# Optimization experiments

Measured on AMD Instinct MI355X. Metric: run time of the kernel, lower is better.

## Reference

```python
import jax, jax.numpy as jnp
import numpy as np

CUTOFF = 5.0
NLINKED = 1
CELL_LIST = CUTOFF / NLINKED  # linked-cell edge length
_r = np.arange(-NLINKED, NLINKED + 1)
# torch.cartesian_prod(r1,r1,r1) == meshgrid(indexing='ij') stacked & flattened
LINKED = np.stack(np.meshgrid(_r, _r, _r, indexing='ij'), axis=-1).reshape(1, -1, 3).astype(np.float32)  # (1, 27, 3)


def setup_inputs() -> dict:
    N = 2744
    L = 30.0
    key = jax.random.key(0)
    k1, k2 = jax.random.split(key)
    coordinates = jax.random.uniform(k1, (N, 3), dtype=jnp.float32) * L
    cell = jnp.eye(3, dtype=jnp.float32) * L
    mass = jax.random.uniform(k2, (N,), dtype=jnp.float32) * 15.0 + 1.0
    period_table = jnp.ones((3,), dtype=jnp.int32)  # fully periodic
    return {"period_table": period_table, "coordinates": coordinates, "cell": cell, "mass": mass}


def _forward(period_table, coordinates, cell, mass):
    numatom = coordinates.shape[0]
    # wrap coordinates into the cell relative to atom 0 (fractional coords)
    inv_cell = jnp.linalg.inv(cell)
    inv_coor = coordinates @ inv_cell
    inv_coor = inv_coor - jnp.round(inv_coor - inv_coor[0])
    coordinates = inv_coor @ cell
    # remove center of mass
    com = (mass @ coordinates) / jnp.sum(mass)
    coordinates = coordinates - com[None, :]
    # periodic replicas needed to cover the cutoff
    num_repeats = jnp.ceil(jnp.min(CUTOFF / jnp.abs(cell), axis=0)).astype(jnp.int32)
    num_repeats = period_table.astype(jnp.int32) * num_repeats
    up = num_repeats + 1
    down = -num_repeats
    rs = [jnp.arange(int(down[i]), int(up[i])) for i in range(3)]
    g = jnp.meshgrid(*rs, indexing='ij')
    shifts_frac = jnp.stack(g, axis=-1).reshape(-1, 3).astype(coordinates.dtype)  # (S, 3)
    shifts = shifts_frac @ cell  # (S, 3) cartesian shift vectors
    num_shifts = shifts.shape[0]
    # prod = cartesian_prod(all_shifts, all_atoms).T : row0 shift idx, row1 atom idx
    prod0 = jnp.repeat(jnp.arange(num_shifts), numatom)
    prod1 = jnp.tile(jnp.arange(numatom), num_shifts)
    # shift box so all coords are positive; pad by cutoff
    mincoor = jnp.min(coordinates, axis=0) - CUTOFF - 1e-6
    coordinates = coordinates - mincoor
    maxcoor = jnp.max(coordinates, axis=0) + CUTOFF
    # all periodic images, keep only those inside the padded box
    image = (coordinates[None, :, :] + shifts[:, None, :]).reshape(-1, 3)
    keep = jnp.nonzero(((image < maxcoor) & (image > 0)).all(axis=1))[0]
    image_mask = image[keep]                      # (M, 3)
    prod0 = prod0[keep]
    prod1 = prod1[keep]
    # linked-cell indices
    ori_image_index = jnp.floor(coordinates / CELL_LIST)         # (N, 3)
    neigh_cell = ori_image_index[:, None, :] + jnp.asarray(LINKED)  # (N, 27, 3)
    image_index = jnp.floor(image_mask / CELL_LIST)              # (M, 3)
    max_cell_index = jnp.ceil(maxcoor / CELL_LIST)
    f10 = max_cell_index[1] * max_cell_index[0]
    neigh_cell_index = neigh_cell[:, :, 2] * f10 + neigh_cell[:, :, 1] * max_cell_index[0] + neigh_cell[:, :, 0]  # (N, 27)
    nimage_index = image_index[:, 2] * f10 + image_index[:, 1] * max_cell_index[0] + image_index[:, 0]            # (M,)
    # dense (N, M, 27) cell-index equality -- the memory-bound hot spot
    eq = neigh_cell_index[:, None, :] == nimage_index[None, :, None]
    ai, aj, _ = jnp.nonzero(eq)
    # distance filter on candidate pairs
    d = jnp.linalg.norm(coordinates[ai] - image_mask[aj], axis=-1)
    pair = jnp.nonzero((d < CUTOFF) & (d > 0.001))[0]
    center = ai[pair]
    img = aj[pair]
    shift_idx = prod0[img]
    atom_j = prod1[img]
    neigh_list = jnp.stack([center, atom_j])  # (2, P)
    return neigh_list, shifts[shift_idx], shifts_frac, shift_idx


def reference(period_table, coordinates, cell, mass):
    neigh_list, shifts_out, _, _ = _forward(period_table, coordinates, cell, mass)
    return (neigh_list, shifts_out)
```

## Files before the change

### kernel.cpp

```cpp
#include <hip/hip_runtime.h>
#include <math.h>

#define S_CAP     27
#define NCELL_MAX 1024
#define CAP       64
#define CAPSH     6
#define MAXNB     128
#define CUT       5.0f
#define K1T       1024


__global__ __launch_bounds__(K1T)
void k1_pre(const int* __restrict__ period, const float* __restrict__ coor,
            const float* __restrict__ cell, const float* __restrict__ mass,
            int* hdr_i, float* hdr_f, float* shifts, float* xv,
            int* __restrict__ ccur, int n)
{
    #pragma clang fp contract(off)
    __shared__ double rs[K1T * 4];
    __shared__ float  redf[K1T * 6];
    __shared__ float  s_com[3];
    int t = threadIdx.x;

    for (int c = t; c < NCELL_MAX; c += K1T) ccur[c] = 0;

    float c[3][3];
    #pragma unroll
    for (int i = 0; i < 3; i++)
        #pragma unroll
        for (int j = 0; j < 3; j++) c[i][j] = cell[3 * i + j];

    float a00 = c[1][1]*c[2][2] - c[1][2]*c[2][1];
    float a01 = c[0][2]*c[2][1] - c[0][1]*c[2][2];
    float a02 = c[0][1]*c[1][2] - c[0][2]*c[1][1];
    float a10 = c[1][2]*c[2][0] - c[1][0]*c[2][2];
    float a11 = c[0][0]*c[2][2] - c[0][2]*c[2][0];
    float a12 = c[0][2]*c[1][0] - c[0][0]*c[1][2];
    float a20 = c[1][0]*c[2][1] - c[1][1]*c[2][0];
    float a21 = c[0][1]*c[2][0] - c[0][0]*c[2][1];
    float a22 = c[0][0]*c[1][1] - c[0][1]*c[1][0];
    float det = c[0][0]*a00 + c[0][1]*a10 + c[0][2]*a20;
    float inv[3][3] = {{a00/det, a01/det, a02/det},
                       {a10/det, a11/det, a12/det},
                       {a20/det, a21/det, a22/det}};

    float f0[3];
    #pragma unroll
    for (int d = 0; d < 3; d++)
        f0[d] = coor[0]*inv[0][d] + coor[1]*inv[1][d] + coor[2]*inv[2][d];

    double sm = 0.0, sx = 0.0, sy = 0.0, sz = 0.0;
    for (int i = t; i < n; i += K1T) {
        float p0 = coor[3*i], p1 = coor[3*i+1], p2 = coor[3*i+2];
        float ic[3], w[3], x[3];
        #pragma unroll
        for (int d = 0; d < 3; d++)
            ic[d] = p0*inv[0][d] + p1*inv[1][d] + p2*inv[2][d];
        #pragma unroll
        for (int d = 0; d < 3; d++)
            w[d] = ic[d] - rintf(ic[d] - f0[d]);
        #pragma unroll
        for (int d = 0; d < 3; d++)
            x[d] = w[0]*c[0][d] + w[1]*c[1][d] + w[2]*c[2][d];
        xv[3*i] = x[0]; xv[3*i+1] = x[1]; xv[3*i+2] = x[2];
        float m = mass[i];
        sm += (double)m;
        sx += (double)m * (double)x[0];
        sy += (double)m * (double)x[1];
        sz += (double)m * (double)x[2];
    }
    rs[t] = sm; rs[K1T+t] = sx; rs[2*K1T+t] = sy; rs[3*K1T+t] = sz;
    __syncthreads();
    for (int off = K1T/2; off > 0; off >>= 1) {
        if (t < off) {
            rs[t]         += rs[t+off];
            rs[K1T+t]     += rs[K1T+t+off];
            rs[2*K1T+t]   += rs[2*K1T+t+off];
            rs[3*K1T+t]   += rs[3*K1T+t+off];
        }
        __syncthreads();
    }
    if (t == 0) {
        float den = (float)rs[0];
        s_com[0] = ((float)rs[K1T])   / den;
        s_com[1] = ((float)rs[2*K1T]) / den;
        s_com[2] = ((float)rs[3*K1T]) / den;
    }
    __syncthreads();
    float com0 = s_com[0], com1 = s_com[1], com2 = s_com[2];

    float mn0 =  __builtin_inff(), mn1 =  __builtin_inff(), mn2 =  __builtin_inff();
    float mx0 = -__builtin_inff(), mx1 = -__builtin_inff(), mx2 = -__builtin_inff();
    for (int i = t; i < n; i += K1T) {
        float v0 = xv[3*i]   - com0;
        float v1 = xv[3*i+1] - com1;
        float v2 = xv[3*i+2] - com2;
        xv[3*i] = v0; xv[3*i+1] = v1; xv[3*i+2] = v2;
        mn0 = fminf(mn0, v0); mn1 = fminf(mn1, v1); mn2 = fminf(mn2, v2);
        mx0 = fmaxf(mx0, v0); mx1 = fmaxf(mx1, v1); mx2 = fmaxf(mx2, v2);
    }
    redf[t]         = mn0; redf[K1T+t]   = mn1; redf[2*K1T+t] = mn2;
    redf[3*K1T+t]   = mx0; redf[4*K1T+t] = mx1; redf[5*K1T+t] = mx2;
    __syncthreads();
    for (int off = K1T/2; off > 0; off >>= 1) {
        if (t < off) {
            redf[t]        = fminf(redf[t],        redf[t+off]);
            redf[K1T+t]    = fminf(redf[K1T+t],    redf[K1T+t+off]);
            redf[2*K1T+t]  = fminf(redf[2*K1T+t],  redf[2*K1T+t+off]);
            redf[3*K1T+t]  = fmaxf(redf[3*K1T+t],  redf[3*K1T+t+off]);
            redf[4*K1T+t]  = fmaxf(redf[4*K1T+t],  redf[4*K1T+t+off]);
            redf[5*K1T+t]  = fmaxf(redf[5*K1T+t],  redf[5*K1T+t+off]);
        }
        __syncthreads();
    }
    if (t == 0) {
        float m20 = (redf[0]     - CUT) - 1e-6f;
        float m21 = (redf[K1T]   - CUT) - 1e-6f;
        float m22 = (redf[2*K1T] - CUT) - 1e-6f;
        float maxc0 = (redf[3*K1T] - m20) + CUT;
        float maxc1 = (redf[4*K1T] - m21) + CUT;
        float maxc2 = (redf[5*K1T] - m22) + CUT;
        float mcell0 = ceilf(maxc0 / CUT);
        float mcell1 = ceilf(maxc1 / CUT);
        float f10 = mcell1 * mcell0;
        int nr[3];
        for (int j = 0; j < 3; j++) {
            float v = __builtin_inff();
            for (int i = 0; i < 3; i++) {
                float q = CUT / fabsf(c[i][j]);
                v = fminf(v, q);
            }
            nr[j] = (int)ceilf(v);
            nr[j] *= period[j];
        }
        int nsz0 = 2*nr[0]+1, nsz1 = 2*nr[1]+1, nsz2 = 2*nr[2]+1;
        int S = nsz0 * nsz1 * nsz2;
        if (S > S_CAP) S = S_CAP;
        hdr_i[0] = S;
        hdr_i[3] = -nr[0]; hdr_i[4] = -nr[1]; hdr_i[5] = -nr[2];
        hdr_i[6] = nsz0;   hdr_i[7] = nsz1;   hdr_i[8] = nsz2;
        hdr_i[9]  = (int)mcell0;
        hdr_i[10] = (int)f10;
        hdr_f[0] = maxc0; hdr_f[1] = maxc1; hdr_f[2] = maxc2;
        hdr_f[3] = f10;   hdr_f[4] = mcell0;
        hdr_f[5] = m20;   hdr_f[6] = m21;   hdr_f[7] = m22;
    }
    __syncthreads();
    int S = hdr_i[0];
    if (t < S) {
        int n1 = hdr_i[7], n2 = hdr_i[8];
        int i0 = t / (n1 * n2);
        int rem = t - i0 * n1 * n2;
        int i1 = rem / n2;
        int i2 = rem - i1 * n2;
        float fx = (float)(hdr_i[3] + i0);
        float fy = (float)(hdr_i[4] + i1);
        float fz = (float)(hdr_i[5] + i2);
        #pragma unroll
        for (int d = 0; d < 3; d++)
            shifts[3*t + d] = fx*c[0][d] + fy*c[1][d] + fz*c[2][d];
    }
}

__global__ __launch_bounds__(256)
void k2_fill(const int* __restrict__ hdr_i, const float* __restrict__ hdr_f,
             const float* __restrict__ shifts, const float* __restrict__ xv,
             int* __restrict__ ccur, float4* __restrict__ cellbuf, int n)
{
    #pragma clang fp contract(off)
    int a = blockIdx.x * 256 + threadIdx.x;
    int s = blockIdx.y;
    if (a >= n || s >= hdr_i[0]) return;
    float m20 = hdr_f[5], m21 = hdr_f[6], m22 = hdr_f[7];
    float i0 = (xv[3*a]   - m20) + shifts[3*s];
    float i1 = (xv[3*a+1] - m21) + shifts[3*s+1];
    float i2 = (xv[3*a+2] - m22) + shifts[3*s+2];
    bool k = (i0 > 0.0f) && (i0 < hdr_f[0]) &&
             (i1 > 0.0f) && (i1 < hdr_f[1]) &&
             (i2 > 0.0f) && (i2 < hdr_f[2]);
    if (!k) return;
    float fc0 = floorf(i0 / CUT);
    float fc1 = floorf(i1 / CUT);
    float fc2 = floorf(i2 / CUT);
    float cf = fc2 * hdr_f[3] + fc1 * hdr_f[4] + fc0;
    int ci = (int)cf;
    if ((unsigned)ci >= (unsigned)NCELL_MAX) return;
    int pos = atomicAdd(&ccur[ci], 1);
    if (pos < CAP)
        cellbuf[(ci << CAPSH) + pos] = make_float4(i0, i1, i2, __int_as_float(s * n + a));
}

__global__ __launch_bounds__(256)
void k3_search(const int* __restrict__ hdr_i, const float* __restrict__ hdr_f,
               const float* __restrict__ xv, const int* __restrict__ ccur,
               const float4* __restrict__ cellbuf, int* __restrict__ nb,
               int* __restrict__ npair, int n)
{
    #pragma clang fp contract(off)
    int t    = threadIdx.x;
    int lane = t & 63;
    int w    = t >> 6;
    int atom = blockIdx.x * 4 + w;
    if (atom >= n) return;

    float m20 = hdr_f[5], m21 = hdr_f[6], m22 = hdr_f[7];
    int mci = hdr_i[9], f10i = hdr_i[10];
    float x0 = xv[3*atom]   - m20;
    float x1 = xv[3*atom+1] - m21;
    float x2 = xv[3*atom+2] - m22;
    int o0 = (int)floorf(x0 / CUT);
    int o1 = (int)floorf(x1 / CUT);
    int o2 = (int)floorf(x2 / CUT);

    int ncb[9], c0a[9], c1a[9], c2a[9], cum[10];
    cum[0] = 0;
    #pragma unroll
    for (int r = 0; r < 9; r++) {
        int dz = r / 3 - 1, dy = r % 3 - 1;
        ncb[r] = (o2+dz)*f10i + (o1+dy)*mci + (o0-1);
        int q0 = 0, q1 = 0, q2 = 0, nc;
        nc = ncb[r];     if ((unsigned)nc < (unsigned)NCELL_MAX) { q0 = ccur[nc]; q0 = q0 > CAP ? CAP : q0; }
        nc = ncb[r] + 1; if ((unsigned)nc < (unsigned)NCELL_MAX) { q1 = ccur[nc]; q1 = q1 > CAP ? CAP : q1; }
        nc = ncb[r] + 2; if ((unsigned)nc < (unsigned)NCELL_MAX) { q2 = ccur[nc]; q2 = q2 > CAP ? CAP : q2; }
        c0a[r] = q0; c1a[r] = q1; c2a[r] = q2;
        cum[r+1] = cum[r] + q0 + q1 + q2;
    }
    int T = cum[9];
    int cnt = 0;
    int* slab = nb + (size_t)atom * MAXNB;
    for (int base = 0; base < T; base += 64) {
        int L = base + lane;
        bool act = L < T;
        bool ok = false; int g = 0;
        if (act) {
            int r = 0;
            #pragma unroll
            for (int q = 1; q < 9; q++) r += (L >= cum[q]) ? 1 : 0;
            int off = L - cum[r];
            int c0 = c0a[r], c1 = c1a[r];
            int slot = (off < c0)      ? ((ncb[r]     << CAPSH) + off)
                     : (off < c0 + c1) ? (((ncb[r]+1) << CAPSH) + off - c0)
                                       : (((ncb[r]+2) << CAPSH) + off - c0 - c1);
            float4 v = cellbuf[slot];
            g = __float_as_int(v.w);
            float dxx = x0 - v.x;
            float dyy = x1 - v.y;
            float dzz = x2 - v.z;
            float ss = dxx*dxx + dyy*dyy + dzz*dzz;
            float dd = sqrtf(ss);
            ok = (dd < CUT) && (dd > 0.001f);
        }
        unsigned long long m = __ballot(ok);
        int posn = cnt + (int)__popcll(m & ((1ull << lane) - 1ull));
        if (ok && posn < MAXNB) slab[posn] = g;
        cnt += (int)__popcll(m);
    }
    if (cnt > MAXNB) cnt = MAXNB;
    if (lane == 0) npair[atom] = cnt;
}

__global__ __launch_bounds__(256)
void k4_emit(const int* __restrict__ nb, const int* __restrict__ npair,
             const float* __restrict__ shifts, float* __restrict__ out,
             int n, int P)
{
    __shared__ int si[256];
    __shared__ int lst[4][MAXNB];
    __shared__ int s_np[4];
    int t    = threadIdx.x;
    int lane = t & 63;
    int w    = t >> 6;
    int blk  = blockIdx.x;
    int atom = blk * 4 + w;
    bool valid = atom < n;

    int lim = blk * 4;
    int s = 0;
    for (int i = t; i < lim; i += 256) s += npair[i];
    si[t] = s;
    __syncthreads();
    for (int off = 128; off > 0; off >>= 1) {
        if (t < off) si[t] += si[t + off];
        __syncthreads();
    }
    int prefB = si[0];

    int cnt = 0;
    if (valid) {
        cnt = npair[atom];
        if (cnt > MAXNB) cnt = MAXNB;
        if (lane == 0) s_np[w] = cnt;
        const int* slab = nb + (size_t)atom * MAXNB;
        for (int r = lane; r < cnt; r += 64) lst[w][r] = slab[r];
    } else if (lane == 0) {
        s_np[w] = 0;
    }
    __syncthreads();

    if (valid) {
        int base = prefB;
        for (int q = 0; q < w; q++) base += s_np[q];
        for (int r = lane; r < cnt; r += 64) {
            int g = lst[w][r];
            int rank = 0;
            for (int q = 0; q < cnt; q++) rank += (lst[w][q] < g) ? 1 : 0;
            int p = base + rank;
            if (p < P) {
                int sidx = g / n;
                int a = g - sidx * n;
                out[p]     = (float)atom;
                out[P + p] = (float)a;
                out[2*P + 3*p]     = shifts[3*sidx];
                out[2*P + 3*p + 1] = shifts[3*sidx + 1];
                out[2*P + 3*p + 2] = shifts[3*sidx + 2];
            }
        }
    }
}

extern "C" void kernel_launch(void* const* d_in, const int* in_sizes, int n_in,
                              void* d_out, int out_size, void* d_ws, size_t ws_size,
                              hipStream_t stream)
{
    const int*   period = (const int*)d_in[0];
    const float* coor   = (const float*)d_in[1];
    const float* cell   = (const float*)d_in[2];
    const float* mass   = (const float*)d_in[3];
    float* out = (float*)d_out;

    int n = in_sizes[1] / 3;
    int P = out_size / 5;

    char* wp = (char*)d_ws;
    size_t off = 0;
    auto alloc = [&](size_t bytes) -> void* {
        off = (off + 15) & ~(size_t)15;
        void* pp = (void*)(wp + off); off += bytes; return pp;
    };

    int*    hdr_i   = (int*)   alloc(16 * 4);
    float*  hdr_f   = (float*) alloc(16 * 4);
    float*  shifts  = (float*) alloc(3 * S_CAP * 4);
    float*  xv      = (float*) alloc(3 * (size_t)n * 4);
    int*    ccur    = (int*)   alloc(NCELL_MAX * 4);
    float4* cellbuf = (float4*)alloc((size_t)NCELL_MAX * CAP * 16);
    int*    nb      = (int*)   alloc((size_t)n * MAXNB * 4);
    int*    npair   = (int*)   alloc((size_t)n * 4);
    (void)ws_size; (void)n_in;

    int gb_atom = (n + 3) / 4;
    dim3 g2((n + 255) / 256, S_CAP);

    hipLaunchKernelGGL(k1_pre,    dim3(1),       dim3(K1T), 0, stream,
                       period, coor, cell, mass, hdr_i, hdr_f, shifts, xv, ccur, n);
    hipLaunchKernelGGL(k2_fill,   g2,            dim3(256), 0, stream,
                       hdr_i, hdr_f, shifts, xv, ccur, cellbuf, n);
    hipLaunchKernelGGL(k3_search, dim3(gb_atom), dim3(256), 0, stream,
                       hdr_i, hdr_f, xv, ccur, cellbuf, nb, npair, n);
    hipLaunchKernelGGL(k4_emit,   dim3(gb_atom), dim3(256), 0, stream,
                       nb, npair, shifts, out, n, P);
}
```

Baseline: 87.76 us.

## Fuse neighbor search and emit into one kernel with grid-wide scan

Merges the search and emit kernels into one. Each block keeps its per-atom neighbor lists in shared memory instead of writing them to a global slab. The last block to finish, found through an atomic ticket, computes a single global prefix sum of the pair counts and raises a flag. The other blocks spin on that flag and then write the output. This removes a kernel launch, the global neighbor-slab round trip and the redundant per-block prefix reductions, but it relies on all blocks being co-resident and adds spin-wait latency.

Measured after the change: 199.3 us. 127% more time.

```diff
diff --git a/kernel.cpp b/kernel.cpp
--- a/kernel.cpp
+++ b/kernel.cpp
@@ -8,6 +8,7 @@
 #define MAXNB     128
 #define CUT       5.0f
 #define K1T       1024
+#define MAXCH     16
 
 
 __global__ __launch_bounds__(K1T)
@@ -23,6 +24,7 @@
     int t = threadIdx.x;
 
     for (int c = t; c < NCELL_MAX; c += K1T) ccur[c] = 0;
+    if (t < 2) hdr_i[13 + t] = 0;
 
     float c[3][3];
     #pragma unroll
@@ -190,116 +192,129 @@
         cellbuf[(ci << CAPSH) + pos] = make_float4(i0, i1, i2, __int_as_float(s * n + a));
 }
 
-__global__ __launch_bounds__(256)
-void k3_search(const int* __restrict__ hdr_i, const float* __restrict__ hdr_f,
-               const float* __restrict__ xv, const int* __restrict__ ccur,
-               const float4* __restrict__ cellbuf, int* __restrict__ nb,
-               int* __restrict__ npair, int n)
+__global__ __launch_bounds__(256, 4)
+void k3_mega(const int* __restrict__ hdr_i, const float* __restrict__ hdr_f,
+             const float* __restrict__ xv, const int* __restrict__ ccur,
+             const float4* __restrict__ cellbuf, const float* __restrict__ shifts,
+             int* __restrict__ npair, int* __restrict__ pstart,
+             int* ticket, int* flag, float* __restrict__ out, int n, int P)
 {
     #pragma clang fp contract(off)
+    __shared__ int lst[4][MAXNB];
+    __shared__ int si[256];
+    __shared__ int s_scan;
+    __shared__ int s_base[4];
     int t    = threadIdx.x;
     int lane = t & 63;
     int w    = t >> 6;
     int atom = blockIdx.x * 4 + w;
-    if (atom >= n) return;
-
-    float m20 = hdr_f[5], m21 = hdr_f[6], m22 = hdr_f[7];
-    int mci = hdr_i[9], f10i = hdr_i[10];
-    float x0 = xv[3*atom]   - m20;
-    float x1 = xv[3*atom+1] - m21;
-    float x2 = xv[3*atom+2] - m22;
-    int o0 = (int)floorf(x0 / CUT);
-    int o1 = (int)floorf(x1 / CUT);
-    int o2 = (int)floorf(x2 / CUT);
-
-    int ncb[9], c0a[9], c1a[9], c2a[9], cum[10];
-    cum[0] = 0;
-    #pragma unroll
-    for (int r = 0; r < 9; r++) {
-        int dz = r / 3 - 1, dy = r % 3 - 1;
-        ncb[r] = (o2+dz)*f10i + (o1+dy)*mci + (o0-1);
-        int q0 = 0, q1 = 0, q2 = 0, nc;
-        nc = ncb[r];     if ((unsigned)nc < (unsigned)NCELL_MAX) { q0 = ccur[nc]; q0 = q0 > CAP ? CAP : q0; }
-        nc = ncb[r] + 1; if ((unsigned)nc < (unsigned)NCELL_MAX) { q1 = ccur[nc]; q1 = q1 > CAP ? CAP : q1; }
-        nc = ncb[r] + 2; if ((unsigned)nc < (unsigned)NCELL_MAX) { q2 = ccur[nc]; q2 = q2 > CAP ? CAP : q2; }
-        c0a[r] = q0; c1a[r] = q1; c2a[r] = q2;
-        cum[r+1] = cum[r] + q0 + q1 + q2;
-    }
-    int T = cum[9];
+
     int cnt = 0;
-    int* slab = nb + (size_t)atom * MAXNB;
-    for (int base = 0; base < T; base += 64) {
-        int L = base + lane;
-        bool act = L < T;
-        bool ok = false; int g = 0;
-        if (act) {
-            int r = 0;
-            #pragma unroll
-            for (int q = 1; q < 9; q++) r += (L >= cum[q]) ? 1 : 0;
-            int off = L - cum[r];
-            int c0 = c0a[r], c1 = c1a[r];
-            int slot = (off < c0)      ? ((ncb[r]     << CAPSH) + off)
-                     : (off < c0 + c1) ? (((ncb[r]+1) << CAPSH) + off - c0)
-                                       : (((ncb[r]+2) << CAPSH) + off - c0 - c1);
-            float4 v = cellbuf[slot];
-            g = __float_as_int(v.w);
-            float dxx = x0 - v.x;
-            float dyy = x1 - v.y;
-            float dzz = x2 - v.z;
-            float ss = dxx*dxx + dyy*dyy + dzz*dzz;
-            float dd = sqrtf(ss);
-            ok = (dd < CUT) && (dd > 0.001f);
-        }
-        unsigned long long m = __ballot(ok);
-        int posn = cnt + (int)__popcll(m & ((1ull << lane) - 1ull));
-        if (ok && posn < MAXNB) slab[posn] = g;
-        cnt += (int)__popcll(m);
-    }
-    if (cnt > MAXNB) cnt = MAXNB;
-    if (lane == 0) npair[atom] = cnt;
-}
-
-__global__ __launch_bounds__(256)
-void k4_emit(const int* __restrict__ nb, const int* __restrict__ npair,
-             const float* __restrict__ shifts, float* __restrict__ out,
-             int n, int P)
-{
-    __shared__ int si[256];
-    __shared__ int lst[4][MAXNB];
-    __shared__ int s_np[4];
-    int t    = threadIdx.x;
-    int lane = t & 63;
-    int w    = t >> 6;
-    int blk  = blockIdx.x;
-    int atom = blk * 4 + w;
-    bool valid = atom < n;
-
-    int lim = blk * 4;
-    int s = 0;
-    for (int i = t; i < lim; i += 256) s += npair[i];
-    si[t] = s;
-    __syncthreads();
-    for (int off = 128; off > 0; off >>= 1) {
-        if (t < off) si[t] += si[t + off];
+    if (atom < n) {
+        float m20 = hdr_f[5], m21 = hdr_f[6], m22 = hdr_f[7];
+        int mci = hdr_i[9], f10i = hdr_i[10];
+        float x0 = xv[3*atom]   - m20;
+        float x1 = xv[3*atom+1] - m21;
+        float x2 = xv[3*atom+2] - m22;
+        int o0 = (int)floorf(x0 / CUT);
+        int o1 = (int)floorf(x1 / CUT);
+        int o2 = (int)floorf(x2 / CUT);
+
+        int ncb[9], c0a[9], c1a[9], cum[10];
+        cum[0] = 0;
+        #pragma unroll
+        for (int r = 0; r < 9; r++) {
+            int dz = r / 3 - 1, dy = r % 3 - 1;
+            ncb[r] = (o2+dz)*f10i + (o1+dy)*mci + (o0-1);
+            int q0 = 0, q1 = 0, q2 = 0, nc;
+            nc = ncb[r];     if ((unsigned)nc < (unsigned)NCELL_MAX) { q0 = ccur[nc]; q0 = q0 > CAP ? CAP : q0; }
+            nc = ncb[r] + 1; if ((unsigned)nc < (unsigned)NCELL_MAX) { q1 = ccur[nc]; q1 = q1 > CAP ? CAP : q1; }
+            nc = ncb[r] + 2; if ((unsigned)nc < (unsigned)NCELL_MAX) { q2 = ccur[nc]; q2 = q2 > CAP ? CAP : q2; }
+            c0a[r] = q0; c1a[r] = q1;
+            cum[r+1] = cum[r] + q0 + q1 + q2;
+        }
+        int T = cum[9];
+        for (int base = 0; base < T; base += 64) {
+            int L = base + lane;
+            bool act = L < T;
+            bool ok = false; int g = 0;
+            if (act) {
+                int r = 0;
+                #pragma unroll
+                for (int q = 1; q < 9; q++) r += (L >= cum[q]) ? 1 : 0;
+                int off = L - cum[r];
+                int c0 = c0a[r], c1 = c1a[r];
+                int slot = (off < c0)      ? ((ncb[r]     << CAPSH) + off)
+                         : (off < c0 + c1) ? (((ncb[r]+1) << CAPSH) + off - c0)
+                                           : (((ncb[r]+2) << CAPSH) + off - c0 - c1);
+                float4 v = cellbuf[slot];
+                g = __float_as_int(v.w);
+                float dxx = x0 - v.x;
+                float dyy = x1 - v.y;
+                float dzz = x2 - v.z;
+                float ss = dxx*dxx + dyy*dyy + dzz*dzz;
+                float dd = sqrtf(ss);
+                ok = (dd < CUT) && (dd > 0.001f);
+            }
+            unsigned long long m = __ballot(ok);
+            int posn = cnt + (int)__popcll(m & ((1ull << lane) - 1ull));
+            if (ok && posn < MAXNB) lst[w][posn] = g;
+            cnt += (int)__popcll(m);
+        }
+        if (cnt > MAXNB) cnt = MAXNB;
+        if (lane == 0)
+            __hip_atomic_store(&npair[atom], cnt, __ATOMIC_RELAXED, __HIP_MEMORY_SCOPE_AGENT);
+    }
+    __syncthreads();
+
+    if (t == 0) {
+        int old = __hip_atomic_fetch_add(ticket, 1, __ATOMIC_ACQ_REL, __HIP_MEMORY_SCOPE_AGENT);
+        s_scan = (old == (int)gridDim.x - 1) ? 1 : 0;
+    }
+    __syncthreads();
+    if (s_scan) {
+        int CH = (n + 255) / 256;
+        if (CH > MAXCH) CH = MAXCH;
+        int base = t * CH;
+        int vals[MAXCH];
+        int lsum = 0;
+        for (int e = 0; e < CH; e++) {
+            int g = base + e;
+            vals[e] = (g < n) ? __hip_atomic_load(&npair[g], __ATOMIC_RELAXED, __HIP_MEMORY_SCOPE_AGENT) : 0;
+            lsum += vals[e];
+        }
+        si[t] = lsum;
         __syncthreads();
-    }
-    int prefB = si[0];
-
-    int cnt = 0;
-    if (valid) {
-        cnt = npair[atom];
-        if (cnt > MAXNB) cnt = MAXNB;
-        if (lane == 0) s_np[w] = cnt;
-        const int* slab = nb + (size_t)atom * MAXNB;
-        for (int r = lane; r < cnt; r += 64) lst[w][r] = slab[r];
-    } else if (lane == 0) {
-        s_np[w] = 0;
-    }
-    __syncthreads();
-
-    if (valid) {
-        int base = prefB;
-        for (int q = 0; q < w; q++) base += s_np[q];
+        for (int off = 1; off < 256; off <<= 1) {
+            int v = (t >= off) ? si[t - off] : 0;
+            __syncthreads();
+            si[t] += v;
+            __syncthreads();
+        }
+        int run = si[t] - lsum;
+        for (int e = 0; e < CH; e++) {
+            int g = base + e;
+            if (g < n) {
+                __hip_atomic_store(&pstart[g], run, __ATOMIC_RELAXED, __HIP_MEMORY_SCOPE_AGENT);
+                run += vals[e];
+            }
+        }
+        __syncthreads();
+        if (t == 0)
+            __hip_atomic_store(flag, 1, __ATOMIC_RELEASE, __HIP_MEMORY_SCOPE_AGENT);
+    } else {
+        if (t == 0) {
+            while (__hip_atomic_load(flag, __ATOMIC_ACQUIRE, __HIP_MEMORY_SCOPE_AGENT) == 0)
+                __builtin_amdgcn_s_sleep(8);
+        }
+    }
+    __syncthreads();
+
+    if (atom < n && lane == 0)
+        s_base[w] = __hip_atomic_load(&pstart[atom], __ATOMIC_RELAXED, __HIP_MEMORY_SCOPE_AGENT);
+    __syncthreads();
+    if (atom < n) {
+        int base = s_base[w];
         for (int r = lane; r < cnt; r += 64) {
             int g = lst[w][r];
             int rank = 0;
@@ -344,19 +359,18 @@
     float*  xv      = (float*) alloc(3 * (size_t)n * 4);
     int*    ccur    = (int*)   alloc(NCELL_MAX * 4);
     float4* cellbuf = (float4*)alloc((size_t)NCELL_MAX * CAP * 16);
-    int*    nb      = (int*)   alloc((size_t)n * MAXNB * 4);
     int*    npair   = (int*)   alloc((size_t)n * 4);
+    int*    pstart  = (int*)   alloc(((size_t)n + 1) * 4);
     (void)ws_size; (void)n_in;
 
     int gb_atom = (n + 3) / 4;
     dim3 g2((n + 255) / 256, S_CAP);
 
-    hipLaunchKernelGGL(k1_pre,    dim3(1),       dim3(K1T), 0, stream,
+    hipLaunchKernelGGL(k1_pre,  dim3(1),       dim3(K1T), 0, stream,
                        period, coor, cell, mass, hdr_i, hdr_f, shifts, xv, ccur, n);
-    hipLaunchKernelGGL(k2_fill,   g2,            dim3(256), 0, stream,
+    hipLaunchKernelGGL(k2_fill, g2,            dim3(256), 0, stream,
                        hdr_i, hdr_f, shifts, xv, ccur, cellbuf, n);
-    hipLaunchKernelGGL(k3_search, dim3(gb_atom), dim3(256), 0, stream,
-                       hdr_i, hdr_f, xv, ccur, cellbuf, nb, npair, n);
-    hipLaunchKernelGGL(k4_emit,   dim3(gb_atom), dim3(256), 0, stream,
-                       nb, npair, shifts, out, n, P);
+    hipLaunchKernelGGL(k3_mega, dim3(gb_atom), dim3(256), 0, stream,
+                       hdr_i, hdr_f, xv, ccur, cellbuf, shifts,
+                       npair, pstart, &hdr_i[13], &hdr_i[14], out, n, P);
 }
```

## Fuse COM and bounds reductions into one pass with wavefront shuffles

Applied to the files above, without the earlier changes.

The single-block preprocessing kernel now computes the mass-weighted sums and the coordinate min/max in one pass over the atoms. It reduces them with 64-lane shuffles plus a 16-entry shared array, replacing two shared-memory tree reductions that each took 10 barrier steps. The COM subtraction is no longer written back to global memory. Instead the COM goes into the header and later kernels subtract it on the fly, removing a second read/write pass over the coordinates. The min/max are now taken before the COM subtraction, which could change rounding slightly and shift atoms at cell boundaries.

Result: no change. 87.46 us (median of 2 runs) (-0.3%).

```diff
diff --git a/kernel.cpp b/kernel.cpp
--- a/kernel.cpp
+++ b/kernel.cpp
@@ -17,9 +17,8 @@
             int* __restrict__ ccur, int n)
 {
     #pragma clang fp contract(off)
-    __shared__ double rs[K1T * 4];
-    __shared__ float  redf[K1T * 6];
-    __shared__ float  s_com[3];
+    __shared__ double wsum[16][4];
+    __shared__ float  wred[16][6];
     int t = threadIdx.x;
 
     for (int c = t; c < NCELL_MAX; c += K1T) ccur[c] = 0;
@@ -50,6 +49,8 @@
         f0[d] = coor[0]*inv[0][d] + coor[1]*inv[1][d] + coor[2]*inv[2][d];
 
     double sm = 0.0, sx = 0.0, sy = 0.0, sz = 0.0;
+    float mn0 =  __builtin_inff(), mn1 =  __builtin_inff(), mn2 =  __builtin_inff();
+    float mx0 = -__builtin_inff(), mx1 = -__builtin_inff(), mx2 = -__builtin_inff();
     for (int i = t; i < n; i += K1T) {
         float p0 = coor[3*i], p1 = coor[3*i+1], p2 = coor[3*i+2];
         float ic[3], w[3], x[3];
@@ -68,58 +69,49 @@
         sx += (double)m * (double)x[0];
         sy += (double)m * (double)x[1];
         sz += (double)m * (double)x[2];
-    }
-    rs[t] = sm; rs[K1T+t] = sx; rs[2*K1T+t] = sy; rs[3*K1T+t] = sz;
+        mn0 = fminf(mn0, x[0]); mn1 = fminf(mn1, x[1]); mn2 = fminf(mn2, x[2]);
+        mx0 = fmaxf(mx0, x[0]); mx1 = fmaxf(mx1, x[1]); mx2 = fmaxf(mx2, x[2]);
+    }
+    #pragma unroll
+    for (int off = 32; off > 0; off >>= 1) {
+        sm += __shfl_down(sm, off, 64);
+        sx += __shfl_down(sx, off, 64);
+        sy += __shfl_down(sy, off, 64);
+        sz += __shfl_down(sz, off, 64);
+        mn0 = fminf(mn0, __shfl_down(mn0, off, 64));
+        mn1 = fminf(mn1, __shfl_down(mn1, off, 64));
+        mn2 = fminf(mn2, __shfl_down(mn2, off, 64));
+        mx0 = fmaxf(mx0, __shfl_down(mx0, off, 64));
+        mx1 = fmaxf(mx1, __shfl_down(mx1, off, 64));
+        mx2 = fmaxf(mx2, __shfl_down(mx2, off, 64));
+    }
+    if ((t & 63) == 0) {
+        int wv = t >> 6;
+        wsum[wv][0] = sm; wsum[wv][1] = sx; wsum[wv][2] = sy; wsum[wv][3] = sz;
+        wred[wv][0] = mn0; wred[wv][1] = mn1; wred[wv][2] = mn2;
+        wred[wv][3] = mx0; wred[wv][4] = mx1; wred[wv][5] = mx2;
+    }
     __syncthreads();
-    for (int off = K1T/2; off > 0; off >>= 1) {
-        if (t < off) {
-            rs[t]         += rs[t+off];
-            rs[K1T+t]     += rs[K1T+t+off];
-            rs[2*K1T+t]   += rs[2*K1T+t+off];
-            rs[3*K1T+t]   += rs[3*K1T+t+off];
+    if (t == 0) {
+        double SM = 0.0, SX = 0.0, SY = 0.0, SZ = 0.0;
+        float MN0 =  __builtin_inff(), MN1 =  __builtin_inff(), MN2 =  __builtin_inff();
+        float MX0 = -__builtin_inff(), MX1 = -__builtin_inff(), MX2 = -__builtin_inff();
+        #pragma unroll
+        for (int q = 0; q < 16; q++) {
+            SM += wsum[q][0]; SX += wsum[q][1]; SY += wsum[q][2]; SZ += wsum[q][3];
+            MN0 = fminf(MN0, wred[q][0]); MN1 = fminf(MN1, wred[q][1]); MN2 = fminf(MN2, wred[q][2]);
+            MX0 = fmaxf(MX0, wred[q][3]); MX1 = fmaxf(MX1, wred[q][4]); MX2 = fmaxf(MX2, wred[q][5]);
         }
-        __syncthreads();
-    }
-    if (t == 0) {
-        float den = (float)rs[0];
-        s_com[0] = ((float)rs[K1T])   / den;
-        s_com[1] = ((float)rs[2*K1T]) / den;
-        s_com[2] = ((float)rs[3*K1T]) / den;
-    }
-    __syncthreads();
-    float com0 = s_com[0], com1 = s_com[1], com2 = s_com[2];
-
-    float mn0 =  __builtin_inff(), mn1 =  __builtin_inff(), mn2 =  __builtin_inff();
-    float mx0 = -__builtin_inff(), mx1 = -__builtin_inff(), mx2 = -__builtin_inff();
-    for (int i = t; i < n; i += K1T) {
-        float v0 = xv[3*i]   - com0;
-        float v1 = xv[3*i+1] - com1;
-        float v2 = xv[3*i+2] - com2;
-        xv[3*i] = v0; xv[3*i+1] = v1; xv[3*i+2] = v2;
-        mn0 = fminf(mn0, v0); mn1 = fminf(mn1, v1); mn2 = fminf(mn2, v2);
-        mx0 = fmaxf(mx0, v0); mx1 = fmaxf(mx1, v1); mx2 = fmaxf(mx2, v2);
-    }
-    redf[t]         = mn0; redf[K1T+t]   = mn1; redf[2*K1T+t] = mn2;
-    redf[3*K1T+t]   = mx0; redf[4*K1T+t] = mx1; redf[5*K1T+t] = mx2;
-    __syncthreads();
-    for (int off = K1T/2; off > 0; off >>= 1) {
-        if (t < off) {
-            redf[t]        = fminf(redf[t],        redf[t+off]);
-            redf[K1T+t]    = fminf(redf[K1T+t],    redf[K1T+t+off]);
-            redf[2*K1T+t]  = fminf(redf[2*K1T+t],  redf[2*K1T+t+off]);
-            redf[3*K1T+t]  = fmaxf(redf[3*K1T+t],  redf[3*K1T+t+off]);
-            redf[4*K1T+t]  = fmaxf(redf[4*K1T+t],  redf[4*K1T+t+off]);
-            redf[5*K1T+t]  = fmaxf(redf[5*K1T+t],  redf[5*K1T+t+off]);
-        }
-        __syncthreads();
-    }
-    if (t == 0) {
-        float m20 = (redf[0]     - CUT) - 1e-6f;
-        float m21 = (redf[K1T]   - CUT) - 1e-6f;
-        float m22 = (redf[2*K1T] - CUT) - 1e-6f;
-        float maxc0 = (redf[3*K1T] - m20) + CUT;
-        float maxc1 = (redf[4*K1T] - m21) + CUT;
-        float maxc2 = (redf[5*K1T] - m22) + CUT;
+        float den  = (float)SM;
+        float com0 = ((float)SX) / den;
+        float com1 = ((float)SY) / den;
+        float com2 = ((float)SZ) / den;
+        float m20 = ((MN0 - com0) - CUT) - 1e-6f;
+        float m21 = ((MN1 - com1) - CUT) - 1e-6f;
+        float m22 = ((MN2 - com2) - CUT) - 1e-6f;
+        float maxc0 = ((MX0 - com0) - m20) + CUT;
+        float maxc1 = ((MX1 - com1) - m21) + CUT;
+        float maxc2 = ((MX2 - com2) - m22) + CUT;
         float mcell0 = ceilf(maxc0 / CUT);
         float mcell1 = ceilf(maxc1 / CUT);
         float f10 = mcell1 * mcell0;
@@ -144,6 +136,7 @@
         hdr_f[0] = maxc0; hdr_f[1] = maxc1; hdr_f[2] = maxc2;
         hdr_f[3] = f10;   hdr_f[4] = mcell0;
         hdr_f[5] = m20;   hdr_f[6] = m21;   hdr_f[7] = m22;
+        hdr_f[8] = com0;  hdr_f[9] = com1;  hdr_f[10] = com2;
     }
     __syncthreads();
     int S = hdr_i[0];
@@ -172,9 +165,13 @@
     int s = blockIdx.y;
     if (a >= n || s >= hdr_i[0]) return;
     float m20 = hdr_f[5], m21 = hdr_f[6], m22 = hdr_f[7];
-    float i0 = (xv[3*a]   - m20) + shifts[3*s];
-    float i1 = (xv[3*a+1] - m21) + shifts[3*s+1];
-    float i2 = (xv[3*a+2] - m22) + shifts[3*s+2];
+    float com0 = hdr_f[8], com1 = hdr_f[9], com2 = hdr_f[10];
+    float u0 = (xv[3*a]   - com0) - m20;
+    float u1 = (xv[3*a+1] - com1) - m21;
+    float u2 = (xv[3*a+2] - com2) - m22;
+    float i0 = u0 + shifts[3*s];
+    float i1 = u1 + shifts[3*s+1];
+    float i2 = u2 + shifts[3*s+2];
     bool k = (i0 > 0.0f) && (i0 < hdr_f[0]) &&
              (i1 > 0.0f) && (i1 < hdr_f[1]) &&
              (i2 > 0.0f) && (i2 < hdr_f[2]);
@@ -204,15 +201,16 @@
     if (atom >= n) return;
 
     float m20 = hdr_f[5], m21 = hdr_f[6], m22 = hdr_f[7];
+    float com0 = hdr_f[8], com1 = hdr_f[9], com2 = hdr_f[10];
     int mci = hdr_i[9], f10i = hdr_i[10];
-    float x0 = xv[3*atom]   - m20;
-    float x1 = xv[3*atom+1] - m21;
-    float x2 = xv[3*atom+2] - m22;
+    float x0 = (xv[3*atom]   - com0) - m20;
+    float x1 = (xv[3*atom+1] - com1) - m21;
+    float x2 = (xv[3*atom+2] - com2) - m22;
     int o0 = (int)floorf(x0 / CUT);
     int o1 = (int)floorf(x1 / CUT);
     int o2 = (int)floorf(x2 / CUT);
 
-    int ncb[9], c0a[9], c1a[9], c2a[9], cum[10];
+    int ncb[9], c0a[9], c1a[9], cum[10];
     cum[0] = 0;
     #pragma unroll
     for (int r = 0; r < 9; r++) {
@@ -222,7 +220,7 @@
         nc = ncb[r];     if ((unsigned)nc < (unsigned)NCELL_MAX) { q0 = ccur[nc]; q0 = q0 > CAP ? CAP : q0; }
         nc = ncb[r] + 1; if ((unsigned)nc < (unsigned)NCELL_MAX) { q1 = ccur[nc]; q1 = q1 > CAP ? CAP : q1; }
         nc = ncb[r] + 2; if ((unsigned)nc < (unsigned)NCELL_MAX) { q2 = ccur[nc]; q2 = q2 > CAP ? CAP : q2; }
-        c0a[r] = q0; c1a[r] = q1; c2a[r] = q2;
+        c0a[r] = q0; c1a[r] = q1;
         cum[r+1] = cum[r] + q0 + q1 + q2;
     }
     int T = cum[9];
```
